# Optimization experiments

Measured on AMD Instinct MI355X. Metric: run time of the kernel, lower is better.

Reference implementation:

```python
import jax, jax.numpy as jnp
import numpy as np

HEADS = 4
DIM_HEAD = 32
EPS = 1e-5


def setup_inputs() -> dict:
    key = jax.random.key(0)
    ks = jax.random.split(key, 4)
    B, C, H, W = 4, 32, 32, 32
    hidden = C * HEADS * DIM_HEAD  # 4096
    image = jax.random.normal(ks[0], (B, C, H, W), dtype=jnp.float32)
    w_qkv = jax.random.normal(ks[1], (3 * hidden, C), dtype=jnp.float32) * (1.0 / np.sqrt(C))
    b_qkv = jnp.zeros((3 * hidden,), dtype=jnp.float32)
    w_out = jax.random.normal(ks[2], (C, hidden), dtype=jnp.float32) * (1.0 / np.sqrt(hidden))
    b_out = jnp.zeros((C,), dtype=jnp.float32)
    gn_gamma = jnp.ones((C,), dtype=jnp.float32)
    gn_beta = jnp.zeros((C,), dtype=jnp.float32)
    return {"image": image, "w_qkv": w_qkv, "b_qkv": b_qkv,
            "w_out": w_out, "b_out": b_out,
            "gn_gamma": gn_gamma, "gn_beta": gn_beta}


def reference(image, w_qkv, b_qkv, w_out, b_out, gn_gamma, gn_beta):
    B, C, H, W = image.shape
    hidden = C * HEADS * DIM_HEAD
    d = hidden // HEADS  # per-head channel dim = C * DIM_HEAD
    N = H * W
    scale = DIM_HEAD ** (-0.5)

    # 1x1 conv to qkv: [B, 3*hidden, H, W]
    qkv = jnp.einsum('bcxy,oc->boxy', image, w_qkv) + b_qkv[None, :, None, None]
    q, k, v = jnp.split(qkv, 3, axis=1)

    # einops 'b (c h) x y -> b h c (x y)': channel index = c*HEADS + h
    def rearr(t):
        return t.reshape(B, d, HEADS, N).transpose(0, 2, 1, 3)  # [B, h, d, N]

    q, k, v = rearr(q), rearr(k), rearr(v)

    q = jax.nn.softmax(q, axis=-2) * scale  # softmax over feature dim d
    k = jax.nn.softmax(k, axis=-1)          # softmax over spatial dim N

    context = jnp.einsum('bhdn,bhen->bhde', k, v)   # [B, h, d, d]
    out = jnp.einsum('bhde,bhdn->bhen', context, q)  # [B, h, d, N]

    # einops 'b h c (x y) -> b (h c) x y'
    out = out.reshape(B, hidden, H, W)

    # 1x1 conv back to channels, then GroupNorm(1, C)
    out = jnp.einsum('bcxy,oc->boxy', out, w_out) + b_out[None, :, None, None]
    mean = out.mean(axis=(1, 2, 3), keepdims=True)
    var = out.var(axis=(1, 2, 3), keepdims=True)
    out = (out - mean) * jax.lax.rsqrt(var + EPS)
    return out * gn_gamma[None, :, None, None] + gn_beta[None, :, None, None]
```

## Files before the change

kernel.cpp:

```cpp
#include <hip/hip_runtime.h>
#include <stdint.h>

#define HID 4096
#define NSP 1024
#define CIN 32

typedef unsigned short u16;
typedef float f32x4 __attribute__((ext_vector_type(4)));
typedef _Float16 f16;
typedef _Float16 f16x8 __attribute__((ext_vector_type(8)));
typedef unsigned short u16x4 __attribute__((ext_vector_type(4)));
typedef unsigned short u16x8 __attribute__((ext_vector_type(8)));

__device__ __forceinline__ u16 f2h(float f) {
  return __builtin_bit_cast(u16, (f16)f);
}
__device__ __forceinline__ float h2f(u16 u) {
  return (float)__builtin_bit_cast(f16, u);
}

__device__ __forceinline__ void gload16(const u16* g, u16* l) {
  __builtin_amdgcn_global_load_lds(
      (const __attribute__((address_space(1))) void*)g,
      (__attribute__((address_space(3))) void*)l, 16, 0, 0);
}

template <int SECBASE, bool DO_EXP>
__global__ __launch_bounds__(256) void conv_kv(const float* __restrict__ img,
    const float* __restrict__ wq, const float* __restrict__ bq,
    u16* __restrict__ out) {
  __shared__ __align__(16) float imgS[32 * 256];
  __shared__ __align__(16) float wS[32 * 64];
  __shared__ float bS[64];
  int t = threadIdx.x;
  int ch0 = blockIdx.x * 64, nt0 = blockIdx.y * 256, b = blockIdx.z;
  int nl = t & 63, cg = t >> 6;
#pragma unroll
  for (int i = 0; i < 8; i++) {
    int idx = t + i * 256;
    *(f32x4*)&imgS[idx * 4] =
        *(const f32x4*)&img[((size_t)b * CIN + (idx >> 6)) * NSP + nt0 + (idx & 63) * 4];
  }
#pragma unroll
  for (int i = 0; i < 8; i++) {
    int idx = t + i * 256;
    int chl = idx >> 5, c = idx & 31;
    wS[c * 64 + chl] = wq[(size_t)(SECBASE + ch0 + chl) * CIN + c];
  }
  if (t < 64) bS[t] = bq[SECBASE + ch0 + t];
  __syncthreads();
  f32x4 acc[16];
#pragma unroll
  for (int i = 0; i < 16; i++) {
    f32x4 zz = {0.f, 0.f, 0.f, 0.f};
    acc[i] = zz;
  }
#pragma unroll
  for (int c = 0; c < 32; c++) {
    f32x4 x = *(const f32x4*)&imgS[c * 256 + nl * 4];
    const f32x4* wv = (const f32x4*)&wS[c * 64 + cg * 16];
#pragma unroll
    for (int g = 0; g < 4; g++) {
      f32x4 w4 = wv[g];
      acc[g * 4 + 0] += w4[0] * x;
      acc[g * 4 + 1] += w4[1] * x;
      acc[g * 4 + 2] += w4[2] * x;
      acc[g * 4 + 3] += w4[3] * x;
    }
  }
#pragma unroll
  for (int i = 0; i < 16; i++) {
    int ch = ch0 + cg * 16 + i;
    float bias = bS[cg * 16 + i];
    u16x4 o;
#pragma unroll
    for (int j = 0; j < 4; j++) {
      float vv = acc[i][j] + bias;
      if constexpr (DO_EXP) vv = __expf(vv);
      o[j] = f2h(vv);
    }
    size_t row = (size_t)(b * 4 + (ch & 3)) * 1024 + (ch >> 2);
    *(u16x4*)&out[row * NSP + nt0 + nl * 4] = o;
  }
}

__global__ __launch_bounds__(256) void conv_q(const float* __restrict__ img,
    const float* __restrict__ wq, const float* __restrict__ bq,
    u16* __restrict__ qt) {
  __shared__ __align__(16) float imgS[32 * 256];
  __shared__ __align__(16) float wS[32 * 64];
  __shared__ float bS[64];
  int t = threadIdx.x;
  int d0 = blockIdx.x * 64, nt0 = blockIdx.y * 256, z = blockIdx.z;
  int b = z >> 2, hh = z & 3;
  int dl = t & 15, ng = t >> 4;
#pragma unroll
  for (int i = 0; i < 8; i++) {
    int idx = t + i * 256;
    *(f32x4*)&imgS[idx * 4] =
        *(const f32x4*)&img[((size_t)b * CIN + (idx >> 6)) * NSP + nt0 + (idx & 63) * 4];
  }
#pragma unroll
  for (int i = 0; i < 8; i++) {
    int idx = t + i * 256;
    int chl = idx >> 5, c = idx & 31;
    wS[c * 64 + chl] = wq[(size_t)((d0 + chl) * 4 + hh) * CIN + c];
  }
  if (t < 64) bS[t] = bq[(d0 + t) * 4 + hh];
  __syncthreads();
  f32x4 acc[16];
#pragma unroll
  for (int i = 0; i < 16; i++) {
    f32x4 zz = {0.f, 0.f, 0.f, 0.f};
    acc[i] = zz;
  }
#pragma unroll
  for (int c = 0; c < 32; c++) {
    f32x4 w4 = *(const f32x4*)&wS[c * 64 + dl * 4];
#pragma unroll
    for (int j = 0; j < 16; j++) {
      float x = imgS[c * 256 + ng + j * 16];
      acc[j] += x * w4;
    }
  }
  f32x4 bb = *(const f32x4*)&bS[dl * 4];
  size_t base = (size_t)z * 1024 * 1024;
#pragma unroll
  for (int j = 0; j < 16; j++) {
    int n = nt0 + ng + j * 16;
    u16x4 o;
#pragma unroll
    for (int q = 0; q < 4; q++) o[q] = f2h(__expf(acc[j][q] + bb[q]));
    *(u16x4*)&qt[base + (size_t)n * 1024 + d0 + dl * 4] = o;
  }
}

__global__ __launch_bounds__(256) void rowinv(const u16* __restrict__ kexp,
    const u16* __restrict__ qtexp, float* __restrict__ kinv,
    float* __restrict__ qinv) {
  int t = threadIdx.x;
  int wv = t >> 6, l = t & 63;
  int row = blockIdx.x * 4 + wv;
  const u16* src = (row < 16384) ? kexp + (size_t)row * 1024
                                 : qtexp + (size_t)(row - 16384) * 1024;
  const u16x8* p = (const u16x8*)(src + l * 16);
  u16x8 a = p[0], bvec = p[1];
  float s = 0.f;
#pragma unroll
  for (int j = 0; j < 8; j++) s += h2f(a[j]) + h2f(bvec[j]);
#pragma unroll
  for (int off = 32; off > 0; off >>= 1) s += __shfl_xor(s, off);
  if (l == 0) {
    s = fmaxf(s, 1e-20f);
    if (row < 16384) kinv[row] = 1.0f / s;
    else qinv[row - 16384] = 0.17677669529663687f / s;
  }
}

template <int MB, bool FIRST>
__device__ __forceinline__ void phase_load(int wm, int wn, int l,
    const u16* ASp, const u16* BSp, f16x8 (&bfr)[4][2], f16x8 (&afr)[2][2]) {
  if constexpr (FIRST) {
#pragma unroll
    for (int n = 0; n < 4; n++) {
      int row = wn * 64 + n * 16 + (l & 15);
#pragma unroll
      for (int ks = 0; ks < 2; ks++) {
        int cjs = (ks * 4 + (l >> 4)) ^ (row & 7);
        bfr[n][ks] = *(const f16x8*)&BSp[row * 64 + cjs * 8];
      }
    }
  }
#pragma unroll
  for (int mm = 0; mm < 2; mm++) {
    int row = wm * 128 + (MB + mm) * 16 + (l & 15);
#pragma unroll
    for (int ks = 0; ks < 2; ks++) {
      int cjs = (ks * 4 + (l >> 4)) ^ (row & 7);
      afr[mm][ks] = *(const f16x8*)&ASp[row * 64 + cjs * 8];
    }
  }
}

template <int MB>
__device__ __forceinline__ void phase_fma(f16x8 (&bfr)[4][2], f16x8 (&afr)[2][2],
                                          f32x4 (&acc)[8][4]) {
  __builtin_amdgcn_s_setprio(1);
#pragma unroll
  for (int n = 0; n < 4; n++) {
#pragma unroll
    for (int mm = 0; mm < 2; mm++) {
      acc[MB + mm][n] = __builtin_amdgcn_mfma_f32_16x16x32_f16(
          afr[mm][0], bfr[n][0], acc[MB + mm][n], 0, 0, 0);
      acc[MB + mm][n] = __builtin_amdgcn_mfma_f32_16x16x32_f16(
          afr[mm][1], bfr[n][1], acc[MB + mm][n], 0, 0, 0);
    }
  }
  __builtin_amdgcn_s_setprio(0);
}

#define SCHED0 __builtin_amdgcn_sched_barrier(0)
#define BARRIER() do { SCHED0; __builtin_amdgcn_s_barrier(); SCHED0; } while (0)

__global__ __launch_bounds__(512, 2) void gemm8(const u16* __restrict__ A0,
    const u16* __restrict__ B0, u16* __restrict__ C0,
    const float* __restrict__ colscale) {
  __shared__ __align__(16) u16 AS[2][256 * 64];
  __shared__ __align__(16) u16 BS[2][256 * 64];
  int t = threadIdx.x;
  int w = t >> 6, l = t & 63;
  int wm = w >> 2, wn = w & 3;
  int bid = blockIdx.x;
  int xcd = bid & 7, rr = bid >> 3;
  int z = ((rr >> 4) << 3) | xcd;
  int ti = rr & 15, by = ti >> 2, bx = ti & 3;
  const u16* Ag = A0 + (size_t)z * (1024 * 1024) + (size_t)by * 256 * 1024;
  const u16* Bg = B0 + (size_t)z * (1024 * 1024) + (size_t)bx * 256 * 1024;

  f32x4 acc[8][4];
#pragma unroll
  for (int m = 0; m < 8; m++)
#pragma unroll
    for (int n = 0; n < 4; n++) {
      f32x4 zz = {0.f, 0.f, 0.f, 0.f};
      acc[m][n] = zz;
    }
  f16x8 bfr[4][2];

  auto stageH = [&](u16* lds, const u16* g, int half, int k0) {
#pragma unroll
    for (int i = 0; i < 2; i++) {
      int cid = i * 512 + t;
      int r = cid >> 3, cj = cid & 7;
      gload16(g + (size_t)(half * 128 + r) * 1024 + k0 + ((cj ^ (r & 7)) * 8),
              lds + (half * 128 + r) * 64 + cj * 8);
    }
  };

  stageH(BS[0], Bg, 0, 0);
  stageH(BS[0], Bg, 1, 0);
  stageH(AS[0], Ag, 0, 0);
  stageH(AS[0], Ag, 1, 0);
  stageH(BS[1], Bg, 0, 64);
  stageH(BS[1], Bg, 1, 64);
  stageH(AS[1], Ag, 0, 64);
  asm volatile("s_waitcnt vmcnt(6)" ::: "memory");
  BARRIER();

  for (int kt = 0; kt < 16; kt++) {
    int pb = kt & 1;
    const u16* ASp = AS[pb];
    const u16* BSp = BS[pb];
    int kN1 = (kt + 1) * 64, kN2 = (kt + 2) * 64;
    f16x8 afr[2][2];
    phase_load<0, true>(wm, wn, l, ASp, BSp, bfr, afr);
    if (kt < 15) stageH(AS[1 - pb], Ag, 1, kN1);
    BARRIER();
    phase_fma<0>(bfr, afr, acc);
    BARRIER();
    phase_load<2, false>(wm, wn, l, ASp, BSp, bfr, afr);
    if (kt < 14) stageH(BS[pb], Bg, 0, kN2);
    BARRIER();
    phase_fma<2>(bfr, afr, acc);
    BARRIER();
    phase_load<4, false>(wm, wn, l, ASp, BSp, bfr, afr);
    if (kt < 14) stageH(BS[pb], Bg, 1, kN2);
    BARRIER();
    phase_fma<4>(bfr, afr, acc);
    BARRIER();
    phase_load<6, false>(wm, wn, l, ASp, BSp, bfr, afr);
    BARRIER();
    phase_fma<6>(bfr, afr, acc);
    BARRIER();
    if (kt < 14) stageH(AS[pb], Ag, 0, kN2);
    if (kt < 15) {
      if (kt == 14) asm volatile("s_waitcnt vmcnt(0)" ::: "memory");
      else          asm volatile("s_waitcnt vmcnt(6)" ::: "memory");
      BARRIER();
    }
  }

  u16* Cp = C0 + (size_t)z * (1024 * 1024);
  const float* csz = colscale + (size_t)z * 1024;
  int rbase = by * 256 + wm * 128 + (l >> 4) * 4;
  int cbase = bx * 256 + wn * 64 + (l & 15);
  float sc[4];
#pragma unroll
  for (int n = 0; n < 4; n++) sc[n] = csz[cbase + n * 16];
#pragma unroll
  for (int m = 0; m < 8; m++)
#pragma unroll
    for (int n = 0; n < 4; n++)
#pragma unroll
      for (int j = 0; j < 4; j++)
        Cp[(size_t)(rbase + m * 16 + j) * 1024 + cbase + n * 16] =
            f2h(acc[m][n][j] * sc[n]);
}

__global__ __launch_bounds__(256) void oproj(const u16* __restrict__ att,
    const float* __restrict__ wout, float* __restrict__ partial) {
  __shared__ __align__(16) float wS[128 * 20];
  int t = threadIdx.x;
  int kc = blockIdx.x, og = blockIdx.y, b = blockIdx.z;
  for (int i = t; i < 128 * 16; i += 256) {
    int cc = i & 127, oo = i >> 7;
    wS[cc * 20 + oo] = wout[(size_t)(og * 16 + oo) * HID + kc * 128 + cc];
  }
  __syncthreads();
  f32x4 acc[16];
#pragma unroll
  for (int o = 0; o < 16; o++) {
    f32x4 zz = {0.f, 0.f, 0.f, 0.f};
    acc[o] = zz;
  }
  const u16* X = att + ((size_t)b * HID + kc * 128) * NSP + t * 4;
#pragma unroll 4
  for (int cc = 0; cc < 128; cc++) {
    u16x4 xr = *(const u16x4*)(X + (size_t)cc * NSP);
    f32x4 x = {h2f(xr[0]), h2f(xr[1]), h2f(xr[2]), h2f(xr[3])};
    const f32x4* wv = (const f32x4*)&wS[cc * 20];
#pragma unroll
    for (int g = 0; g < 4; g++) {
      f32x4 w4 = wv[g];
      acc[g * 4 + 0] += w4[0] * x;
      acc[g * 4 + 1] += w4[1] * x;
      acc[g * 4 + 2] += w4[2] * x;
      acc[g * 4 + 3] += w4[3] * x;
    }
  }
#pragma unroll
  for (int o = 0; o < 16; o++)
    *(f32x4*)&partial[(((size_t)b * 32 + kc) * 32 + og * 16 + o) * NSP + t * 4] = acc[o];
}

__global__ __launch_bounds__(256) void reduce_stats(const float* __restrict__ partial,
    const float* __restrict__ bout, float* __restrict__ fin,
    float* __restrict__ stats) {
  int t = threadIdx.x;
  int gid = blockIdx.x * 256 + t;
  int n = gid & 1023;
  int o = (gid >> 10) & 31;
  int b = gid >> 15;
  const float* p = partial + ((size_t)b * 32 * 32 + o) * NSP + n;
  float v[32];
#pragma unroll
  for (int kc = 0; kc < 32; kc++) v[kc] = p[(size_t)kc * 32 * NSP];
  float s = bout[o];
#pragma unroll
  for (int kc = 0; kc < 32; kc++) s += v[kc];
  fin[((size_t)b * 32 + o) * NSP + n] = s;
  float s1 = s, s2 = s * s;
#pragma unroll
  for (int off = 32; off > 0; off >>= 1) {
    s1 += __shfl_xor(s1, off);
    s2 += __shfl_xor(s2, off);
  }
  __shared__ float r1[4], r2[4];
  int wid = t >> 6;
  if ((t & 63) == 0) { r1[wid] = s1; r2[wid] = s2; }
  __syncthreads();
  if (t == 0) {
    stats[blockIdx.x * 2 + 0] = r1[0] + r1[1] + r1[2] + r1[3];
    stats[blockIdx.x * 2 + 1] = r2[0] + r2[1] + r2[2] + r2[3];
  }
}

__global__ __launch_bounds__(256) void gn_norm(const float* __restrict__ fin,
    const float* __restrict__ stats, const float* __restrict__ gamma,
    const float* __restrict__ beta, float* __restrict__ out) {
  int t = threadIdx.x;
  int nc = blockIdx.x, b = blockIdx.y;
  float s1 = 0.f, s2 = 0.f;
  for (int i = 0; i < 128; i++) {
    s1 += stats[(b * 128 + i) * 2 + 0];
    s2 += stats[(b * 128 + i) * 2 + 1];
  }
  const float inv_n = 1.0f / 32768.0f;
  float mean = s1 * inv_n;
  float var = s2 * inv_n - mean * mean;
  float rstd = rsqrtf(var + 1e-5f);
  int nl = t & 63, oq = t >> 6;
  int n = nc * 64 + nl;
#pragma unroll
  for (int oo = 0; oo < 8; oo++) {
    int o = oq * 8 + oo;
    float v = fin[((size_t)b * 32 + o) * NSP + n];
    out[((size_t)b * 32 + o) * NSP + n] = (v - mean) * rstd * gamma[o] + beta[o];
  }
}

extern "C" void kernel_launch(void* const* d_in, const int* in_sizes, int n_in,
                              void* d_out, int out_size, void* d_ws, size_t ws_size,
                              hipStream_t stream) {
  (void)in_sizes; (void)n_in; (void)out_size; (void)ws_size;
  const float* img   = (const float*)d_in[0];
  const float* wqkv  = (const float*)d_in[1];
  const float* bqkv  = (const float*)d_in[2];
  const float* wout  = (const float*)d_in[3];
  const float* bout  = (const float*)d_in[4];
  const float* gamma = (const float*)d_in[5];
  const float* beta  = (const float*)d_in[6];
  char* ws = (char*)d_ws;
  u16*   v       = (u16*)(ws + 0);
  u16*   att     = (u16*)(ws + 0);
  u16*   kexp    = (u16*)(ws + 33554432);
  u16*   qtexp   = (u16*)(ws + 67108864);
  u16*   ctx     = (u16*)(ws + 100663296);
  float* stats   = (float*)(ws + 100663296);
  float* partial = (float*)(ws + 134217728);
  float* kinv    = (float*)(ws + 134217728);
  float* qinv    = (float*)(ws + 134283264);
  float* fin     = (float*)(ws + 150994944);
  float* out = (float*)d_out;

  conv_kv<2 * HID, false><<<dim3(64, 4, 4), 256, 0, stream>>>(img, wqkv, bqkv, v);
  conv_kv<1 * HID, true ><<<dim3(64, 4, 4), 256, 0, stream>>>(img, wqkv, bqkv, kexp);
  conv_q<<<dim3(16, 4, 16), 256, 0, stream>>>(img, wqkv, bqkv, qtexp);
  rowinv<<<dim3(8192), 256, 0, stream>>>(kexp, qtexp, kinv, qinv);
  gemm8<<<dim3(256), 512, 0, stream>>>(v, kexp, ctx, kinv);
  gemm8<<<dim3(256), 512, 0, stream>>>(ctx, qtexp, att, qinv);
  oproj<<<dim3(32, 2, 4), 256, 0, stream>>>(att, wout, partial);
  reduce_stats<<<dim3(512), 256, 0, stream>>>(partial, bout, fin, stats);
  gn_norm<<<dim3(16, 4), 256, 0, stream>>>(fin, stats, gamma, beta, out);
}
```

Measured before the change: 206.0 us.

## Fuse qkv convolutions into one launch and compute softmax sums via atomics

Merges the three 1x1 convolution kernels into a single launch that branches on blockIdx.z. The separate rowinv pass is removed; each conv block now accumulates the exp sums for k and q rows with wave shuffles and atomicAdd into zeroed buffers. The GEMM epilogues compute the reciprocal and scale themselves. This avoids re-reading 64MB of fp16 exp data and saves launches, at the cost of a memset, atomic contention and sums taken in fp32 before rounding to fp16.

```diff
diff --git a/kernel.cpp b/kernel.cpp
--- a/kernel.cpp
+++ b/kernel.cpp
@@ -25,135 +25,132 @@
       (__attribute__((address_space(3))) void*)l, 16, 0, 0);
 }
 
-template <int SECBASE, bool DO_EXP>
-__global__ __launch_bounds__(256) void conv_kv(const float* __restrict__ img,
+__global__ __launch_bounds__(256) void conv_fused(const float* __restrict__ img,
     const float* __restrict__ wq, const float* __restrict__ bq,
-    u16* __restrict__ out) {
+    u16* __restrict__ v, u16* __restrict__ kexp, u16* __restrict__ qtexp,
+    float* __restrict__ ksum, float* __restrict__ qsum) {
   __shared__ __align__(16) float imgS[32 * 256];
   __shared__ __align__(16) float wS[32 * 64];
   __shared__ float bS[64];
   int t = threadIdx.x;
-  int ch0 = blockIdx.x * 64, nt0 = blockIdx.y * 256, b = blockIdx.z;
-  int nl = t & 63, cg = t >> 6;
-#pragma unroll
-  for (int i = 0; i < 8; i++) {
-    int idx = t + i * 256;
-    *(f32x4*)&imgS[idx * 4] =
-        *(const f32x4*)&img[((size_t)b * CIN + (idx >> 6)) * NSP + nt0 + (idx & 63) * 4];
-  }
-#pragma unroll
-  for (int i = 0; i < 8; i++) {
-    int idx = t + i * 256;
-    int chl = idx >> 5, c = idx & 31;
-    wS[c * 64 + chl] = wq[(size_t)(SECBASE + ch0 + chl) * CIN + c];
-  }
-  if (t < 64) bS[t] = bq[SECBASE + ch0 + t];
-  __syncthreads();
-  f32x4 acc[16];
-#pragma unroll
-  for (int i = 0; i < 16; i++) {
-    f32x4 zz = {0.f, 0.f, 0.f, 0.f};
-    acc[i] = zz;
-  }
-#pragma unroll
-  for (int c = 0; c < 32; c++) {
-    f32x4 x = *(const f32x4*)&imgS[c * 256 + nl * 4];
-    const f32x4* wv = (const f32x4*)&wS[c * 64 + cg * 16];
-#pragma unroll
-    for (int g = 0; g < 4; g++) {
-      f32x4 w4 = wv[g];
-      acc[g * 4 + 0] += w4[0] * x;
-      acc[g * 4 + 1] += w4[1] * x;
-      acc[g * 4 + 2] += w4[2] * x;
-      acc[g * 4 + 3] += w4[3] * x;
-    }
-  }
-#pragma unroll
-  for (int i = 0; i < 16; i++) {
-    int ch = ch0 + cg * 16 + i;
-    float bias = bS[cg * 16 + i];
-    u16x4 o;
-#pragma unroll
-    for (int j = 0; j < 4; j++) {
-      float vv = acc[i][j] + bias;
-      if constexpr (DO_EXP) vv = __expf(vv);
-      o[j] = f2h(vv);
-    }
-    size_t row = (size_t)(b * 4 + (ch & 3)) * 1024 + (ch >> 2);
-    *(u16x4*)&out[row * NSP + nt0 + nl * 4] = o;
-  }
-}
-
-__global__ __launch_bounds__(256) void conv_q(const float* __restrict__ img,
-    const float* __restrict__ wq, const float* __restrict__ bq,
-    u16* __restrict__ qt) {
-  __shared__ __align__(16) float imgS[32 * 256];
-  __shared__ __align__(16) float wS[32 * 64];
-  __shared__ float bS[64];
-  int t = threadIdx.x;
-  int d0 = blockIdx.x * 64, nt0 = blockIdx.y * 256, z = blockIdx.z;
-  int b = z >> 2, hh = z & 3;
-  int dl = t & 15, ng = t >> 4;
-#pragma unroll
-  for (int i = 0; i < 8; i++) {
-    int idx = t + i * 256;
-    *(f32x4*)&imgS[idx * 4] =
-        *(const f32x4*)&img[((size_t)b * CIN + (idx >> 6)) * NSP + nt0 + (idx & 63) * 4];
-  }
-#pragma unroll
-  for (int i = 0; i < 8; i++) {
-    int idx = t + i * 256;
-    int chl = idx >> 5, c = idx & 31;
-    wS[c * 64 + chl] = wq[(size_t)((d0 + chl) * 4 + hh) * CIN + c];
-  }
-  if (t < 64) bS[t] = bq[(d0 + t) * 4 + hh];
-  __syncthreads();
-  f32x4 acc[16];
-#pragma unroll
-  for (int i = 0; i < 16; i++) {
-    f32x4 zz = {0.f, 0.f, 0.f, 0.f};
-    acc[i] = zz;
-  }
-#pragma unroll
-  for (int c = 0; c < 32; c++) {
-    f32x4 w4 = *(const f32x4*)&wS[c * 64 + dl * 4];
+  int zz = blockIdx.z;
+
+  if (zz < 8) {
+    bool doexp = (zz >= 4);
+    int b = zz & 3;
+    int sec = doexp ? HID : 2 * HID;
+    u16* outp = doexp ? kexp : v;
+    int ch0 = blockIdx.x * 64, nt0 = blockIdx.y * 256;
+    int nl = t & 63, cg = t >> 6;
+#pragma unroll
+    for (int i = 0; i < 8; i++) {
+      int idx = t + i * 256;
+      *(f32x4*)&imgS[idx * 4] =
+          *(const f32x4*)&img[((size_t)b * CIN + (idx >> 6)) * NSP + nt0 + (idx & 63) * 4];
+    }
+#pragma unroll
+    for (int i = 0; i < 8; i++) {
+      int idx = t + i * 256;
+      int chl = idx >> 5, c = idx & 31;
+      wS[c * 64 + chl] = wq[(size_t)(sec + ch0 + chl) * CIN + c];
+    }
+    if (t < 64) bS[t] = bq[sec + ch0 + t];
+    __syncthreads();
+    f32x4 acc[16];
+#pragma unroll
+    for (int i = 0; i < 16; i++) {
+      f32x4 zzv = {0.f, 0.f, 0.f, 0.f};
+      acc[i] = zzv;
+    }
+#pragma unroll
+    for (int c = 0; c < 32; c++) {
+      f32x4 x = *(const f32x4*)&imgS[c * 256 + nl * 4];
+      const f32x4* wv = (const f32x4*)&wS[c * 64 + cg * 16];
+#pragma unroll
+      for (int g = 0; g < 4; g++) {
+        f32x4 w4 = wv[g];
+        acc[g * 4 + 0] += w4[0] * x;
+        acc[g * 4 + 1] += w4[1] * x;
+        acc[g * 4 + 2] += w4[2] * x;
+        acc[g * 4 + 3] += w4[3] * x;
+      }
+    }
+#pragma unroll
+    for (int i = 0; i < 16; i++) {
+      int ch = ch0 + cg * 16 + i;
+      float bias = bS[cg * 16 + i];
+      u16x4 o;
+      float ss = 0.f;
+#pragma unroll
+      for (int j = 0; j < 4; j++) {
+        float vv = acc[i][j] + bias;
+        if (doexp) vv = __expf(vv);
+        o[j] = f2h(vv);
+        ss += vv;
+      }
+      size_t row = (size_t)(b * 4 + (ch & 3)) * 1024 + (ch >> 2);
+      *(u16x4*)&outp[row * NSP + nt0 + nl * 4] = o;
+      if (doexp) {
+#pragma unroll
+        for (int off = 32; off > 0; off >>= 1) ss += __shfl_xor(ss, off);
+        if (nl == 0) atomicAdd(&ksum[row], ss);
+      }
+    }
+  } else {
+    int x = blockIdx.x, y = blockIdx.y;
+    int bh = (zz - 8) * 4 + (x >> 4);
+    int d0 = (x & 15) * 64, nt0 = y * 256;
+    int b = bh >> 2, hh = bh & 3;
+    int dl = t & 15, ng = t >> 4;
+#pragma unroll
+    for (int i = 0; i < 8; i++) {
+      int idx = t + i * 256;
+      *(f32x4*)&imgS[idx * 4] =
+          *(const f32x4*)&img[((size_t)b * CIN + (idx >> 6)) * NSP + nt0 + (idx & 63) * 4];
+    }
+#pragma unroll
+    for (int i = 0; i < 8; i++) {
+      int idx = t + i * 256;
+      int chl = idx >> 5, c = idx & 31;
+      wS[c * 64 + chl] = wq[(size_t)((d0 + chl) * 4 + hh) * CIN + c];
+    }
+    if (t < 64) bS[t] = bq[(d0 + t) * 4 + hh];
+    __syncthreads();
+    f32x4 acc[16];
+#pragma unroll
+    for (int i = 0; i < 16; i++) {
+      f32x4 zzv = {0.f, 0.f, 0.f, 0.f};
+      acc[i] = zzv;
+    }
+#pragma unroll
+    for (int c = 0; c < 32; c++) {
+      f32x4 w4 = *(const f32x4*)&wS[c * 64 + dl * 4];
+#pragma unroll
+      for (int j = 0; j < 16; j++) {
+        float xv = imgS[c * 256 + ng + j * 16];
+        acc[j] += xv * w4;
+      }
+    }
+    f32x4 bb = *(const f32x4*)&bS[dl * 4];
+    size_t base = (size_t)bh * 1024 * 1024;
 #pragma unroll
     for (int j = 0; j < 16; j++) {
-      float x = imgS[c * 256 + ng + j * 16];
-      acc[j] += x * w4;
-    }
-  }
-  f32x4 bb = *(const f32x4*)&bS[dl * 4];
-  size_t base = (size_t)z * 1024 * 1024;
-#pragma unroll
-  for (int j = 0; j < 16; j++) {
-    int n = nt0 + ng + j * 16;
-    u16x4 o;
-#pragma unroll
-    for (int q = 0; q < 4; q++) o[q] = f2h(__expf(acc[j][q] + bb[q]));
-    *(u16x4*)&qt[base + (size_t)n * 1024 + d0 + dl * 4] = o;
-  }
-}
-
-__global__ __launch_bounds__(256) void rowinv(const u16* __restrict__ kexp,
-    const u16* __restrict__ qtexp, float* __restrict__ kinv,
-    float* __restrict__ qinv) {
-  int t = threadIdx.x;
-  int wv = t >> 6, l = t & 63;
-  int row = blockIdx.x * 4 + wv;
-  const u16* src = (row < 16384) ? kexp + (size_t)row * 1024
-                                 : qtexp + (size_t)(row - 16384) * 1024;
-  const u16x8* p = (const u16x8*)(src + l * 16);
-  u16x8 a = p[0], bvec = p[1];
-  float s = 0.f;
-#pragma unroll
-  for (int j = 0; j < 8; j++) s += h2f(a[j]) + h2f(bvec[j]);
-#pragma unroll
-  for (int off = 32; off > 0; off >>= 1) s += __shfl_xor(s, off);
-  if (l == 0) {
-    s = fmaxf(s, 1e-20f);
-    if (row < 16384) kinv[row] = 1.0f / s;
-    else qinv[row - 16384] = 0.17677669529663687f / s;
+      int n = nt0 + ng + j * 16;
+      u16x4 o;
+      float ss = 0.f;
+#pragma unroll
+      for (int q = 0; q < 4; q++) {
+        float ev = __expf(acc[j][q] + bb[q]);
+        o[q] = f2h(ev);
+        ss += ev;
+      }
+      *(u16x4*)&qtexp[base + (size_t)n * 1024 + d0 + dl * 4] = o;
+      ss += __shfl_xor(ss, 1);
+      ss += __shfl_xor(ss, 2);
+      ss += __shfl_xor(ss, 4);
+      ss += __shfl_xor(ss, 8);
+      if (dl == 0) atomicAdd(&qsum[bh * 1024 + n], ss);
+    }
   }
 }
 
@@ -204,7 +201,7 @@
 
 __global__ __launch_bounds__(512, 2) void gemm8(const u16* __restrict__ A0,
     const u16* __restrict__ B0, u16* __restrict__ C0,
-    const float* __restrict__ colscale) {
+    const float* __restrict__ colsum, float scalemul) {
   __shared__ __align__(16) u16 AS[2][256 * 64];
   __shared__ __align__(16) u16 BS[2][256 * 64];
   int t = threadIdx.x;
@@ -281,12 +278,13 @@
   }
 
   u16* Cp = C0 + (size_t)z * (1024 * 1024);
-  const float* csz = colscale + (size_t)z * 1024;
+  const float* csz = colsum + (size_t)z * 1024;
   int rbase = by * 256 + wm * 128 + (l >> 4) * 4;
   int cbase = bx * 256 + wn * 64 + (l & 15);
   float sc[4];
 #pragma unroll
-  for (int n = 0; n < 4; n++) sc[n] = csz[cbase + n * 16];
+  for (int n = 0; n < 4; n++)
+    sc[n] = scalemul / fmaxf(csz[cbase + n * 16], 1e-10f);
 #pragma unroll
   for (int m = 0; m < 8; m++)
 #pragma unroll
@@ -408,17 +406,17 @@
   u16*   ctx     = (u16*)(ws + 100663296);
   float* stats   = (float*)(ws + 100663296);
   float* partial = (float*)(ws + 134217728);
-  float* kinv    = (float*)(ws + 134217728);
-  float* qinv    = (float*)(ws + 134283264);
+  float* ksum    = (float*)(ws + 134217728);
+  float* qsum    = (float*)(ws + 134283264);
   float* fin     = (float*)(ws + 150994944);
   float* out = (float*)d_out;
 
-  conv_kv<2 * HID, false><<<dim3(64, 4, 4), 256, 0, stream>>>(img, wqkv, bqkv, v);
-  conv_kv<1 * HID, true ><<<dim3(64, 4, 4), 256, 0, stream>>>(img, wqkv, bqkv, kexp);
-  conv_q<<<dim3(16, 4, 16), 256, 0, stream>>>(img, wqkv, bqkv, qtexp);
-  rowinv<<<dim3(8192), 256, 0, stream>>>(kexp, qtexp, kinv, qinv);
-  gemm8<<<dim3(256), 512, 0, stream>>>(v, kexp, ctx, kinv);
-  gemm8<<<dim3(256), 512, 0, stream>>>(ctx, qtexp, att, qinv);
+  hipMemsetAsync(ws + 134217728, 0, 131072, stream);
+  conv_fused<<<dim3(64, 4, 12), 256, 0, stream>>>(img, wqkv, bqkv, v, kexp,
+                                                  qtexp, ksum, qsum);
+  gemm8<<<dim3(256), 512, 0, stream>>>(v, kexp, ctx, ksum, 1.0f);
+  gemm8<<<dim3(256), 512, 0, stream>>>(ctx, qtexp, att, qsum,
+                                       0.17677669529663687f);
   oproj<<<dim3(32, 2, 4), 256, 0, stream>>>(att, wout, partial);
   reduce_stats<<<dim3(512), 256, 0, stream>>>(partial, bout, fin, stats);
   gn_norm<<<dim3(16, 4), 256, 0, stream>>>(fin, stats, gamma, beta, out);
```

New measurement: 529.3 us. +157.0%, slower.

## Merge V/K conv launches, loop oproj output groups, store partials in fp16

Applied to the files above, without the earlier changes.

The two templated conv launches for V and K are combined into one launch that picks the section through blockIdx.z. oproj now loops over both output-channel groups inside one block, so each block reuses its att rows from cache instead of two blocks reading them. Its split-K partial sums are written as fp16 rather than fp32, which halves partial-buffer traffic in oproj and reduce_stats. The costs are precision loss in the partial sums before GroupNorm and half as many oproj blocks, which lowers parallelism.

```diff
diff --git a/kernel.cpp b/kernel.cpp
--- a/kernel.cpp
+++ b/kernel.cpp
@@ -25,15 +25,19 @@
       (__attribute__((address_space(3))) void*)l, 16, 0, 0);
 }
 
-template <int SECBASE, bool DO_EXP>
-__global__ __launch_bounds__(256) void conv_kv(const float* __restrict__ img,
+__global__ __launch_bounds__(256) void conv_vk(const float* __restrict__ img,
     const float* __restrict__ wq, const float* __restrict__ bq,
-    u16* __restrict__ out) {
+    u16* __restrict__ v, u16* __restrict__ kexp) {
   __shared__ __align__(16) float imgS[32 * 256];
   __shared__ __align__(16) float wS[32 * 64];
   __shared__ float bS[64];
   int t = threadIdx.x;
-  int ch0 = blockIdx.x * 64, nt0 = blockIdx.y * 256, b = blockIdx.z;
+  int zz = blockIdx.z;
+  bool doexp = zz >= 4;
+  int b = zz & 3;
+  int sec = doexp ? HID : 2 * HID;
+  u16* outp = doexp ? kexp : v;
+  int ch0 = blockIdx.x * 64, nt0 = blockIdx.y * 256;
   int nl = t & 63, cg = t >> 6;
 #pragma unroll
   for (int i = 0; i < 8; i++) {
@@ -45,15 +49,15 @@
   for (int i = 0; i < 8; i++) {
     int idx = t + i * 256;
     int chl = idx >> 5, c = idx & 31;
-    wS[c * 64 + chl] = wq[(size_t)(SECBASE + ch0 + chl) * CIN + c];
-  }
-  if (t < 64) bS[t] = bq[SECBASE + ch0 + t];
+    wS[c * 64 + chl] = wq[(size_t)(sec + ch0 + chl) * CIN + c];
+  }
+  if (t < 64) bS[t] = bq[sec + ch0 + t];
   __syncthreads();
   f32x4 acc[16];
 #pragma unroll
   for (int i = 0; i < 16; i++) {
-    f32x4 zz = {0.f, 0.f, 0.f, 0.f};
-    acc[i] = zz;
+    f32x4 zv = {0.f, 0.f, 0.f, 0.f};
+    acc[i] = zv;
   }
 #pragma unroll
   for (int c = 0; c < 32; c++) {
@@ -76,11 +80,11 @@
 #pragma unroll
     for (int j = 0; j < 4; j++) {
       float vv = acc[i][j] + bias;
-      if constexpr (DO_EXP) vv = __expf(vv);
+      if (doexp) vv = __expf(vv);
       o[j] = f2h(vv);
     }
     size_t row = (size_t)(b * 4 + (ch & 3)) * 1024 + (ch >> 2);
-    *(u16x4*)&out[row * NSP + nt0 + nl * 4] = o;
+    *(u16x4*)&outp[row * NSP + nt0 + nl * 4] = o;
   }
 }
 
@@ -111,8 +115,8 @@
   f32x4 acc[16];
 #pragma unroll
   for (int i = 0; i < 16; i++) {
-    f32x4 zz = {0.f, 0.f, 0.f, 0.f};
-    acc[i] = zz;
+    f32x4 zv = {0.f, 0.f, 0.f, 0.f};
+    acc[i] = zv;
   }
 #pragma unroll
   for (int c = 0; c < 32; c++) {
@@ -298,42 +302,49 @@
 }
 
 __global__ __launch_bounds__(256) void oproj(const u16* __restrict__ att,
-    const float* __restrict__ wout, float* __restrict__ partial) {
+    const float* __restrict__ wout, u16* __restrict__ partial) {
   __shared__ __align__(16) float wS[128 * 20];
   int t = threadIdx.x;
-  int kc = blockIdx.x, og = blockIdx.y, b = blockIdx.z;
-  for (int i = t; i < 128 * 16; i += 256) {
-    int cc = i & 127, oo = i >> 7;
-    wS[cc * 20 + oo] = wout[(size_t)(og * 16 + oo) * HID + kc * 128 + cc];
-  }
-  __syncthreads();
-  f32x4 acc[16];
-#pragma unroll
-  for (int o = 0; o < 16; o++) {
-    f32x4 zz = {0.f, 0.f, 0.f, 0.f};
-    acc[o] = zz;
-  }
+  int kc = blockIdx.x, b = blockIdx.y;
   const u16* X = att + ((size_t)b * HID + kc * 128) * NSP + t * 4;
+  for (int og = 0; og < 2; og++) {
+    __syncthreads();
+    for (int i = t; i < 128 * 16; i += 256) {
+      int cc = i & 127, oo = i >> 7;
+      wS[cc * 20 + oo] = wout[(size_t)(og * 16 + oo) * HID + kc * 128 + cc];
+    }
+    __syncthreads();
+    f32x4 acc[16];
+#pragma unroll
+    for (int o = 0; o < 16; o++) {
+      f32x4 zz = {0.f, 0.f, 0.f, 0.f};
+      acc[o] = zz;
+    }
 #pragma unroll 4
-  for (int cc = 0; cc < 128; cc++) {
-    u16x4 xr = *(const u16x4*)(X + (size_t)cc * NSP);
-    f32x4 x = {h2f(xr[0]), h2f(xr[1]), h2f(xr[2]), h2f(xr[3])};
-    const f32x4* wv = (const f32x4*)&wS[cc * 20];
-#pragma unroll
-    for (int g = 0; g < 4; g++) {
-      f32x4 w4 = wv[g];
-      acc[g * 4 + 0] += w4[0] * x;
-      acc[g * 4 + 1] += w4[1] * x;
-      acc[g * 4 + 2] += w4[2] * x;
-      acc[g * 4 + 3] += w4[3] * x;
-    }
-  }
-#pragma unroll
-  for (int o = 0; o < 16; o++)
-    *(f32x4*)&partial[(((size_t)b * 32 + kc) * 32 + og * 16 + o) * NSP + t * 4] = acc[o];
-}
-
-__global__ __launch_bounds__(256) void reduce_stats(const float* __restrict__ partial,
+    for (int cc = 0; cc < 128; cc++) {
+      u16x4 xr = *(const u16x4*)(X + (size_t)cc * NSP);
+      f32x4 x = {h2f(xr[0]), h2f(xr[1]), h2f(xr[2]), h2f(xr[3])};
+      const f32x4* wv = (const f32x4*)&wS[cc * 20];
+#pragma unroll
+      for (int g = 0; g < 4; g++) {
+        f32x4 w4 = wv[g];
+        acc[g * 4 + 0] += w4[0] * x;
+        acc[g * 4 + 1] += w4[1] * x;
+        acc[g * 4 + 2] += w4[2] * x;
+        acc[g * 4 + 3] += w4[3] * x;
+      }
+    }
+#pragma unroll
+    for (int o = 0; o < 16; o++) {
+      u16x4 st;
+#pragma unroll
+      for (int j = 0; j < 4; j++) st[j] = f2h(acc[o][j]);
+      *(u16x4*)&partial[(((size_t)b * 32 + kc) * 32 + og * 16 + o) * NSP + t * 4] = st;
+    }
+  }
+}
+
+__global__ __launch_bounds__(256) void reduce_stats(const u16* __restrict__ partial,
     const float* __restrict__ bout, float* __restrict__ fin,
     float* __restrict__ stats) {
   int t = threadIdx.x;
@@ -341,10 +352,10 @@
   int n = gid & 1023;
   int o = (gid >> 10) & 31;
   int b = gid >> 15;
-  const float* p = partial + ((size_t)b * 32 * 32 + o) * NSP + n;
+  const u16* p = partial + ((size_t)b * 32 * 32 + o) * NSP + n;
   float v[32];
 #pragma unroll
-  for (int kc = 0; kc < 32; kc++) v[kc] = p[(size_t)kc * 32 * NSP];
+  for (int kc = 0; kc < 32; kc++) v[kc] = h2f(p[(size_t)kc * 32 * NSP]);
   float s = bout[o];
 #pragma unroll
   for (int kc = 0; kc < 32; kc++) s += v[kc];
@@ -407,19 +418,18 @@
   u16*   qtexp   = (u16*)(ws + 67108864);
   u16*   ctx     = (u16*)(ws + 100663296);
   float* stats   = (float*)(ws + 100663296);
-  float* partial = (float*)(ws + 134217728);
+  u16*   partial = (u16*)(ws + 134217728);
   float* kinv    = (float*)(ws + 134217728);
   float* qinv    = (float*)(ws + 134283264);
   float* fin     = (float*)(ws + 150994944);
   float* out = (float*)d_out;
 
-  conv_kv<2 * HID, false><<<dim3(64, 4, 4), 256, 0, stream>>>(img, wqkv, bqkv, v);
-  conv_kv<1 * HID, true ><<<dim3(64, 4, 4), 256, 0, stream>>>(img, wqkv, bqkv, kexp);
+  conv_vk<<<dim3(64, 4, 8), 256, 0, stream>>>(img, wqkv, bqkv, v, kexp);
   conv_q<<<dim3(16, 4, 16), 256, 0, stream>>>(img, wqkv, bqkv, qtexp);
   rowinv<<<dim3(8192), 256, 0, stream>>>(kexp, qtexp, kinv, qinv);
   gemm8<<<dim3(256), 512, 0, stream>>>(v, kexp, ctx, kinv);
   gemm8<<<dim3(256), 512, 0, stream>>>(ctx, qtexp, att, qinv);
-  oproj<<<dim3(32, 2, 4), 256, 0, stream>>>(att, wout, partial);
+  oproj<<<dim3(32, 4), 256, 0, stream>>>(att, wout, partial);
   reduce_stats<<<dim3(512), 256, 0, stream>>>(partial, bout, fin, stats);
   gn_norm<<<dim3(16, 4), 256, 0, stream>>>(fin, stats, gamma, beta, out);
 }
```

New measurement: 219.6 us. +6.6%, slower.
